# Performance work log

Measured on AMD Instinct MI355X. Metric: run time of the kernel, lower is better.

## Reference

```python
import jax, jax.numpy as jnp
import numpy as np

BATCH = 65536
SEQ_LEN = 32
EMB = 64
H = 128


def setup_inputs() -> dict:
    key = jax.random.key(0)
    ks = jax.random.split(key, 12)
    s = 0.05
    inp = {
        "last_pos": jax.random.normal(ks[0], (BATCH, 2), jnp.float32),
        "last_pos_rel": jax.random.normal(ks[1], (BATCH, 2), jnp.float32),
        "hh": jax.random.normal(ks[2], (1, BATCH, H), jnp.float32),
        "ch": jax.random.normal(ks[3], (1, BATCH, H), jnp.float32),
        "seq_start_end": jnp.sort(jax.random.randint(ks[4], (256, 2), 0, BATCH), axis=0),
        # LSTM(embedding_dim -> h_dim), PyTorch gate order [i, f, g, o]
        "w_ih": jax.random.normal(ks[5], (4 * H, EMB), jnp.float32) * s,
        "w_hh": jax.random.normal(ks[6], (4 * H, H), jnp.float32) * s,
        "b_ih": jax.random.normal(ks[7], (4 * H,), jnp.float32) * s,
        "b_hh": jax.random.normal(ks[8], (4 * H,), jnp.float32) * s,
        # spatial_embedding: Linear(2 -> EMB)
        "w_emb": jax.random.normal(ks[9], (EMB, 2), jnp.float32) * s,
        "b_emb": jax.random.normal(ks[10], (EMB,), jnp.float32) * s,
        # hidden2pos: Linear(H -> 2)
        "w_pos": jax.random.normal(ks[11], (2, H), jnp.float32) * s,
        "b_pos": jnp.zeros((2,), jnp.float32),
    }
    return inp


def _decode(last_pos, last_pos_rel, hh, ch, w_ih, w_hh, b_ih, b_hh,
            w_emb, b_emb, w_pos, b_pos):
    h0, c0 = hh[0], ch[0]                      # (B, H)
    x0 = last_pos_rel @ w_emb.T + b_emb        # (B, EMB)
    b = b_ih + b_hh

    def step(carry, _):
        h, c, lp, x = carry
        gates = x @ w_ih.T + h @ w_hh.T + b    # (B, 4H)
        i, f, g, o = jnp.split(gates, 4, axis=-1)
        c2 = jax.nn.sigmoid(f) * c + jax.nn.sigmoid(i) * jnp.tanh(g)
        h2 = jax.nn.sigmoid(o) * jnp.tanh(c2)
        rel = h2 @ w_pos.T + b_pos             # (B, 2)
        cur = rel + lp
        x2 = rel @ w_emb.T + b_emb             # next decoder input embedding
        return (h2, c2, cur, x2), rel

    (hN, cN, _, _), rels = jax.lax.scan(step, (h0, c0, last_pos, x0),
                                        None, length=SEQ_LEN)
    # rels: (SEQ_LEN, B, 2) == pred_traj_fake_rel; hN[None]: (1, B, H)
    return rels, hN[None]


def reference(last_pos, last_pos_rel, hh, ch, seq_start_end,
              w_ih, w_hh, b_ih, b_hh, w_emb, b_emb, w_pos, b_pos):
    # seq_start_end is unused when pool_every_timestep=False
    return _decode(last_pos, last_pos_rel, hh, ch,
                   w_ih, w_hh, b_ih, b_hh, w_emb, b_emb, w_pos, b_pos)
```

## Files before the change

kernel.cpp:

```cpp
#include <hip/hip_runtime.h>

#define B_TOT 65536
#define SEQ   32

typedef __bf16 bf16_8 __attribute__((ext_vector_type(8)));
typedef __bf16 bf16_4 __attribute__((ext_vector_type(4)));
typedef float  float4v __attribute__((ext_vector_type(4)));
typedef float  float2v __attribute__((ext_vector_type(2)));

#define SC1 (-1.4426950408889634f)
#define SC2 (-2.8853900817779268f)

__device__ inline unsigned short f2bf(float f){
    unsigned u = __builtin_bit_cast(unsigned, f);
    u += 0x7FFFu + ((u >> 16) & 1u);
    return (unsigned short)(u >> 16);
}

__global__ void prep_kernel(const float* __restrict__ w_ih,
                            const float* __restrict__ w_hh,
                            const float* __restrict__ b_ih,
                            const float* __restrict__ b_hh,
                            const float* __restrict__ w_emb,
                            const float* __restrict__ b_emb,
                            const float* __restrict__ w_pos,
                            const float* __restrict__ b_pos,
                            unsigned short* __restrict__ weff,
                            float* __restrict__ beff,
                            float* __restrict__ m2,
                            unsigned short* __restrict__ wposA)
{
    int n = threadIdx.x;
    float m20 = 0.f, m21 = 0.f, bi = 0.f;
    for (int e = 0; e < 64; ++e){
        float wv = w_ih[n*64 + e];
        m20 += w_emb[e*2 + 0] * wv;
        m21 += w_emb[e*2 + 1] * wv;
        bi  += b_emb[e] * wv;
    }
    float sc = ((n >> 7) == 2) ? SC2 : SC1;
    m2[n]       = m20 * sc;
    m2[512 + n] = m21 * sc;
    beff[n] = (b_ih[n] + b_hh[n] + bi + b_pos[0]*m20 + b_pos[1]*m21) * sc;
    for (int k = 0; k < 128; ++k){
        float wv = w_hh[n*128 + k] + w_pos[k]*m20 + w_pos[128 + k]*m21;
        weff[n*128 + k] = f2bf(wv * sc);
    }
    if (n < 256) wposA[n] = f2bf(w_pos[n]);
    for (int idx = n; idx < 14*128; idx += 512) wposA[256 + idx] = 0;
}

__global__ __launch_bounds__(512, 4) void dec_kernel(
    const float* __restrict__ lpr,
    const float* __restrict__ hh,
    const float* __restrict__ ch,
    const float* __restrict__ b_pos,
    const unsigned short* __restrict__ wposA,
    const unsigned short* __restrict__ weff,
    const float* __restrict__ beff,
    const float* __restrict__ m2,
    float* __restrict__ out,
    int tmask)
{
    __shared__ __align__(16) unsigned short lh[2][16][128];
    __shared__ __align__(16) unsigned short wposS[16*128];
    __shared__ float ubuf[16][2];

    const int tid  = threadIdx.x;
    const int w    = tid >> 6;
    const int lane = tid & 63;
    const int q    = lane >> 4;
    const int l    = lane & 15;
    const int row0 = blockIdx.x << 4;
    const int batch = row0 + l;
    const int hb   = w << 4;

    *(uint2*)&wposS[tid << 2] = *(const uint2*)(wposA + (tid << 2));
    {
        int r = tid >> 5, c = (tid & 31) << 2;
        float4v v = *(const float4v*)(hh + ((row0 + r) << 7) + c);
        bf16_4 hv;
        hv[0]=(__bf16)v[0]; hv[1]=(__bf16)v[1]; hv[2]=(__bf16)v[2]; hv[3]=(__bf16)v[3];
        int pcol = ((((c >> 3) ^ r) << 3)) | (c & 7);
        *(bf16_4*)&lh[0][r][pcol] = hv;
    }

    bf16_8 wA[4][4];
#pragma unroll
    for (int g = 0; g < 4; ++g){
        int gr = (g << 7) + hb + l;
#pragma unroll
        for (int kt = 0; kt < 4; ++kt)
            wA[g][kt] = *(const bf16_8*)(weff + (gr << 7) + kt*32 + (q << 3));
    }
    float4v bias4[4];
#pragma unroll
    for (int g = 0; g < 4; ++g)
        bias4[g] = *(const float4v*)(beff + (g << 7) + hb + (q << 2));
    float4v cst = *(const float4v*)(ch + (batch << 7) + hb + (q << 2));
    const float bp0 = b_pos[0], bp1 = b_pos[1];

    __syncthreads();

    float4v acc[4];

    auto fused = [&](int t, bool store_rel) -> float4v {
        const int rbuf = t & 1;
        const bool duty = (w == (t & 7));
        float4v r = {0.f, 0.f, 0.f, 0.f};
#pragma unroll
        for (int kt = 0; kt < 4; ++kt){
            int pcol = (((kt << 2) | q) ^ l) << 3;
            bf16_8 bc = *(const bf16_8*)&lh[rbuf][l][pcol];
            if (kt == 0){
#pragma unroll
                for (int g = 0; g < 4; ++g)
                    acc[g] = __builtin_amdgcn_mfma_f32_16x16x32_bf16(wA[g][0], bc, bias4[g], 0, 0, 0);
            } else {
#pragma unroll
                for (int g = 0; g < 4; ++g)
                    acc[g] = __builtin_amdgcn_mfma_f32_16x16x32_bf16(wA[g][kt], bc, acc[g], 0, 0, 0);
            }
            if (duty){
                bf16_8 wpc = *(const bf16_8*)&wposS[(l << 7) + kt*32 + (q << 3) + (t & tmask)];
                r = __builtin_amdgcn_mfma_f32_16x16x32_bf16(wpc, bc, r, 0, 0, 0);
            }
        }
        if (duty && store_rel && q == 0){
            float2v rv; rv[0] = r[0] + bp0; rv[1] = r[1] + bp1;
            *(float2v*)(out + (t - 1)*(B_TOT*2) + (batch << 1)) = rv;
        }
        return r;
    };

    auto elemwise = [&](int wbuf, bool finalh){
        bf16_4 hv; float4v hf;
#pragma unroll
        for (int r4 = 0; r4 < 4; ++r4){
            float ei = __builtin_amdgcn_exp2f(acc[0][r4]);
            float ef = __builtin_amdgcn_exp2f(acc[1][r4]);
            float eg = __builtin_amdgcn_exp2f(acc[2][r4]);
            float pi_ = 1.f + ei, pf = 1.f + ef;
            float pg  = 1.f + eg, mg = 1.f - eg;
            float t2  = pi_ * pg;
            float den = pf * t2;
            float num = fmaf(cst[r4], t2, pf * mg);
            float c2  = num * __builtin_amdgcn_rcpf(den);
            float eo  = __builtin_amdgcn_exp2f(acc[3][r4]);
            float ec  = __builtin_amdgcn_exp2f(c2 * SC2);
            float po = 1.f + eo, pc = 1.f + ec, mc = 1.f - ec;
            float h2 = mc * __builtin_amdgcn_rcpf(po * pc);
            cst[r4] = c2;
            hv[r4] = (__bf16)h2;
            hf[r4] = h2;
        }
        int pcol = ((((w << 1) | (q >> 1)) ^ l) << 3) | ((q & 1) << 2);
        *(bf16_4*)&lh[wbuf][l][pcol] = hv;
        if (finalh)
            *(float4v*)(out + SEQ*B_TOT*2 + (batch << 7) + hb + (q << 2)) = hf;
    };

    {
        float4v r0 = fused(0, false);
        if (w == 0 && q == 0){
            float2v lp = *(const float2v*)(lpr + (batch << 1));
            ubuf[l][0] = lp[0] - (r0[0] + bp0);
            ubuf[l][1] = lp[1] - (r0[1] + bp1);
        }
        __syncthreads();
        float u0 = ubuf[l][0], u1 = ubuf[l][1];
#pragma unroll
        for (int g = 0; g < 4; ++g){
            int g0 = (g << 7) + hb + (q << 2);
            float4v ma = *(const float4v*)(m2 + g0);
            float4v mb = *(const float4v*)(m2 + 512 + g0);
#pragma unroll
            for (int r4 = 0; r4 < 4; ++r4)
                acc[g][r4] += u0*ma[r4] + u1*mb[r4];
        }
        elemwise(1, false);
        __syncthreads();
    }

#pragma unroll 1
    for (int t = 1; t < SEQ; ++t){
        fused(t, true);
        elemwise((t + 1) & 1, t == SEQ - 1);
        __syncthreads();
    }

    if (w == 0){
        float4v r = {0.f, 0.f, 0.f, 0.f};
#pragma unroll
        for (int kt = 0; kt < 4; ++kt){
            int pcol = (((kt << 2) | q) ^ l) << 3;
            bf16_8 bc = *(const bf16_8*)&lh[0][l][pcol];
            bf16_8 wpc = *(const bf16_8*)&wposS[(l << 7) + kt*32 + (q << 3)];
            r = __builtin_amdgcn_mfma_f32_16x16x32_bf16(wpc, bc, r, 0, 0, 0);
        }
        if (q == 0){
            float2v rv; rv[0] = r[0] + bp0; rv[1] = r[1] + bp1;
            *(float2v*)(out + (SEQ - 1)*(B_TOT*2) + (batch << 1)) = rv;
        }
    }
}

extern "C" void kernel_launch(void* const* d_in, const int* in_sizes, int n_in,
                              void* d_out, int out_size, void* d_ws, size_t ws_size,
                              hipStream_t stream)
{
    (void)in_sizes; (void)n_in; (void)out_size; (void)ws_size;

    const float* lpr   = (const float*)d_in[1];
    const float* hh    = (const float*)d_in[2];
    const float* ch    = (const float*)d_in[3];
    const float* w_ih  = (const float*)d_in[5];
    const float* w_hh  = (const float*)d_in[6];
    const float* b_ih  = (const float*)d_in[7];
    const float* b_hh  = (const float*)d_in[8];
    const float* w_emb = (const float*)d_in[9];
    const float* b_emb = (const float*)d_in[10];
    const float* w_pos = (const float*)d_in[11];
    const float* b_pos = (const float*)d_in[12];

    unsigned short* weff  = (unsigned short*)d_ws;
    float* beff           = (float*)((char*)d_ws + 131072);
    float* m2             = (float*)((char*)d_ws + 131072 + 2048);
    unsigned short* wposA = (unsigned short*)((char*)d_ws + 131072 + 2048 + 4096);

    hipLaunchKernelGGL(prep_kernel, dim3(1), dim3(512), 0, stream,
                       w_ih, w_hh, b_ih, b_hh, w_emb, b_emb, w_pos, b_pos,
                       weff, beff, m2, wposA);
    hipLaunchKernelGGL(dec_kernel, dim3(B_TOT/16), dim3(512), 0, stream,
                       lpr, hh, ch, b_pos, wposA, weff, beff, m2,
                       (float*)d_out, 0);
}
```

Measured before the change: 594.9 us.

## Process two 16-row batch tiles per block to reuse register-resident weights

```diff
diff --git a/kernel.cpp b/kernel.cpp
--- a/kernel.cpp
+++ b/kernel.cpp
@@ -50,7 +50,7 @@
     for (int idx = n; idx < 14*128; idx += 512) wposA[256 + idx] = 0;
 }
 
-__global__ __launch_bounds__(512, 4) void dec_kernel(
+__global__ __launch_bounds__(512, 2) void dec_kernel(
     const float* __restrict__ lpr,
     const float* __restrict__ hh,
     const float* __restrict__ ch,
@@ -59,30 +59,37 @@
     const unsigned short* __restrict__ weff,
     const float* __restrict__ beff,
     const float* __restrict__ m2,
-    float* __restrict__ out,
-    int tmask)
+    float* __restrict__ out)
 {
-    __shared__ __align__(16) unsigned short lh[2][16][128];
-    __shared__ __align__(16) unsigned short wposS[16*128];
-    __shared__ float ubuf[16][2];
+    __shared__ __align__(16) unsigned short lh[2][2][16][128];
+    __shared__ __align__(16) unsigned short wposS[16][136];
+    __shared__ float ubuf[32][2];
 
     const int tid  = threadIdx.x;
     const int w    = tid >> 6;
     const int lane = tid & 63;
     const int q    = lane >> 4;
     const int l    = lane & 15;
-    const int row0 = blockIdx.x << 4;
-    const int batch = row0 + l;
+    const int row0 = blockIdx.x << 5;
+    const int batchA = row0 + l;
+    const int batchB = row0 + 16 + l;
     const int hb   = w << 4;
 
-    *(uint2*)&wposS[tid << 2] = *(const uint2*)(wposA + (tid << 2));
     {
-        int r = tid >> 5, c = (tid & 31) << 2;
-        float4v v = *(const float4v*)(hh + ((row0 + r) << 7) + c);
-        bf16_4 hv;
-        hv[0]=(__bf16)v[0]; hv[1]=(__bf16)v[1]; hv[2]=(__bf16)v[2]; hv[3]=(__bf16)v[3];
-        int pcol = ((((c >> 3) ^ r) << 3)) | (c & 7);
-        *(bf16_4*)&lh[0][r][pcol] = hv;
+        int idx = tid << 2;
+        *(uint2*)&wposS[idx >> 7][idx & 127] = *(const uint2*)(wposA + idx);
+    }
+    {
+        int r = tid >> 4, c = (tid & 15) << 3;
+        const float* ph = hh + ((row0 + r) << 7) + c;
+        float4v v0 = *(const float4v*)ph;
+        float4v v1 = *(const float4v*)(ph + 4);
+        bf16_8 hv;
+        hv[0]=(__bf16)v0[0]; hv[1]=(__bf16)v0[1]; hv[2]=(__bf16)v0[2]; hv[3]=(__bf16)v0[3];
+        hv[4]=(__bf16)v1[0]; hv[5]=(__bf16)v1[1]; hv[6]=(__bf16)v1[2]; hv[7]=(__bf16)v1[3];
+        int rl = r & 15;
+        int pcol = ((c >> 3) ^ rl) << 3;
+        *(bf16_8*)&lh[r >> 4][0][rl][pcol] = hv;
     }
 
     bf16_8 wA[4][4];
@@ -97,21 +104,27 @@
 #pragma unroll
     for (int g = 0; g < 4; ++g)
         bias4[g] = *(const float4v*)(beff + (g << 7) + hb + (q << 2));
-    float4v cst = *(const float4v*)(ch + (batch << 7) + hb + (q << 2));
     const float bp0 = b_pos[0], bp1 = b_pos[1];
 
+    float4v cstA = *(const float4v*)(ch + (batchA << 7) + hb + (q << 2));
+    float4v cstB = *(const float4v*)(ch + (batchB << 7) + hb + (q << 2));
+
     __syncthreads();
 
-    float4v acc[4];
-
-    auto fused = [&](int t, bool store_rel) -> float4v {
-        const int rbuf = t & 1;
-        const bool duty = (w == (t & 7));
+    bf16_8 wp[4];
+#pragma unroll
+    for (int kt = 0; kt < 4; ++kt)
+        wp[kt] = *(const bf16_8*)&wposS[l][kt*32 + (q << 3)];
+
+    float4v accA[4], accB[4];
+
+    auto fused = [&](float4v (&acc)[4], const unsigned short (*tile)[128],
+                     bool duty) -> float4v {
         float4v r = {0.f, 0.f, 0.f, 0.f};
 #pragma unroll
         for (int kt = 0; kt < 4; ++kt){
             int pcol = (((kt << 2) | q) ^ l) << 3;
-            bf16_8 bc = *(const bf16_8*)&lh[rbuf][l][pcol];
+            bf16_8 bc = *(const bf16_8*)&tile[l][pcol];
             if (kt == 0){
 #pragma unroll
                 for (int g = 0; g < 4; ++g)
@@ -121,19 +134,14 @@
                 for (int g = 0; g < 4; ++g)
                     acc[g] = __builtin_amdgcn_mfma_f32_16x16x32_bf16(wA[g][kt], bc, acc[g], 0, 0, 0);
             }
-            if (duty){
-                bf16_8 wpc = *(const bf16_8*)&wposS[(l << 7) + kt*32 + (q << 3) + (t & tmask)];
-                r = __builtin_amdgcn_mfma_f32_16x16x32_bf16(wpc, bc, r, 0, 0, 0);
-            }
-        }
-        if (duty && store_rel && q == 0){
-            float2v rv; rv[0] = r[0] + bp0; rv[1] = r[1] + bp1;
-            *(float2v*)(out + (t - 1)*(B_TOT*2) + (batch << 1)) = rv;
+            if (duty)
+                r = __builtin_amdgcn_mfma_f32_16x16x32_bf16(wp[kt], bc, r, 0, 0, 0);
         }
         return r;
     };
 
-    auto elemwise = [&](int wbuf, bool finalh){
+    auto elemwise = [&](float4v (&acc)[4], float4v& cst,
+                        unsigned short (*tile)[128], bool finalh, int batch){
         bf16_4 hv; float4v hf;
 #pragma unroll
         for (int r4 = 0; r4 < 4; ++r4){
@@ -155,52 +163,69 @@
             hf[r4] = h2;
         }
         int pcol = ((((w << 1) | (q >> 1)) ^ l) << 3) | ((q & 1) << 2);
-        *(bf16_4*)&lh[wbuf][l][pcol] = hv;
+        *(bf16_4*)&tile[l][pcol] = hv;
         if (finalh)
             *(float4v*)(out + SEQ*B_TOT*2 + (batch << 7) + hb + (q << 2)) = hf;
     };
 
     {
-        float4v r0 = fused(0, false);
+        float4v rA = fused(accA, lh[0][0], w == 0);
+        float4v rB = fused(accB, lh[1][0], w == 0);
         if (w == 0 && q == 0){
-            float2v lp = *(const float2v*)(lpr + (batch << 1));
-            ubuf[l][0] = lp[0] - (r0[0] + bp0);
-            ubuf[l][1] = lp[1] - (r0[1] + bp1);
+            float2v lpA = *(const float2v*)(lpr + (batchA << 1));
+            float2v lpB = *(const float2v*)(lpr + (batchB << 1));
+            ubuf[l][0]      = lpA[0] - (rA[0] + bp0);
+            ubuf[l][1]      = lpA[1] - (rA[1] + bp1);
+            ubuf[16 + l][0] = lpB[0] - (rB[0] + bp0);
+            ubuf[16 + l][1] = lpB[1] - (rB[1] + bp1);
         }
         __syncthreads();
-        float u0 = ubuf[l][0], u1 = ubuf[l][1];
+        float uA0 = ubuf[l][0], uA1 = ubuf[l][1];
+        float uB0 = ubuf[16 + l][0], uB1 = ubuf[16 + l][1];
 #pragma unroll
         for (int g = 0; g < 4; ++g){
             int g0 = (g << 7) + hb + (q << 2);
             float4v ma = *(const float4v*)(m2 + g0);
             float4v mb = *(const float4v*)(m2 + 512 + g0);
 #pragma unroll
-            for (int r4 = 0; r4 < 4; ++r4)
-                acc[g][r4] += u0*ma[r4] + u1*mb[r4];
-        }
-        elemwise(1, false);
+            for (int r4 = 0; r4 < 4; ++r4){
+                accA[g][r4] += uA0*ma[r4] + uA1*mb[r4];
+                accB[g][r4] += uB0*ma[r4] + uB1*mb[r4];
+            }
+        }
+        elemwise(accA, cstA, lh[0][1], false, batchA);
+        elemwise(accB, cstB, lh[1][1], false, batchB);
         __syncthreads();
     }
 
 #pragma unroll 1
     for (int t = 1; t < SEQ; ++t){
-        fused(t, true);
-        elemwise((t + 1) & 1, t == SEQ - 1);
+        const bool duty = (w == (t & 7));
+        float4v rA = fused(accA, lh[0][t & 1], duty);
+        float4v rB = fused(accB, lh[1][t & 1], duty);
+        if (duty && q == 0){
+            float2v rvA; rvA[0] = rA[0] + bp0; rvA[1] = rA[1] + bp1;
+            float2v rvB; rvB[0] = rB[0] + bp0; rvB[1] = rB[1] + bp1;
+            *(float2v*)(out + (t - 1)*(B_TOT*2) + (batchA << 1)) = rvA;
+            *(float2v*)(out + (t - 1)*(B_TOT*2) + (batchB << 1)) = rvB;
+        }
+        elemwise(accA, cstA, lh[0][(t + 1) & 1], t == SEQ - 1, batchA);
+        elemwise(accB, cstB, lh[1][(t + 1) & 1], t == SEQ - 1, batchB);
         __syncthreads();
     }
 
-    if (w == 0){
+    if (w < 2){
+        const unsigned short (*tile)[128] = lh[w][0];
         float4v r = {0.f, 0.f, 0.f, 0.f};
 #pragma unroll
         for (int kt = 0; kt < 4; ++kt){
             int pcol = (((kt << 2) | q) ^ l) << 3;
-            bf16_8 bc = *(const bf16_8*)&lh[0][l][pcol];
-            bf16_8 wpc = *(const bf16_8*)&wposS[(l << 7) + kt*32 + (q << 3)];
-            r = __builtin_amdgcn_mfma_f32_16x16x32_bf16(wpc, bc, r, 0, 0, 0);
+            bf16_8 bc = *(const bf16_8*)&tile[l][pcol];
+            r = __builtin_amdgcn_mfma_f32_16x16x32_bf16(wp[kt], bc, r, 0, 0, 0);
         }
         if (q == 0){
             float2v rv; rv[0] = r[0] + bp0; rv[1] = r[1] + bp1;
-            *(float2v*)(out + (SEQ - 1)*(B_TOT*2) + (batch << 1)) = rv;
+            *(float2v*)(out + (SEQ - 1)*(B_TOT*2) + ((row0 + (w << 4) + l) << 1)) = rv;
         }
     }
 }
@@ -231,7 +256,7 @@
     hipLaunchKernelGGL(prep_kernel, dim3(1), dim3(512), 0, stream,
                        w_ih, w_hh, b_ih, b_hh, w_emb, b_emb, w_pos, b_pos,
                        weff, beff, m2, wposA);
-    hipLaunchKernelGGL(dec_kernel, dim3(B_TOT/16), dim3(512), 0, stream,
+    hipLaunchKernelGGL(dec_kernel, dim3(B_TOT/32), dim3(512), 0, stream,
                        lpr, hh, ch, b_pos, wposA, weff, beff, m2,
-                       (float*)d_out, 0);
-}
+                       (float*)d_out);
+}
```

Result: faster. 534.1 us (-10.2%).
